# Performance work log

Hardware: AMD Instinct MI355X
Metric: run time of the kernel (lower is better)

The kernel has to match this reference:

```python
import jax, jax.numpy as jnp
import numpy as np

B, S, H, KV, D = 1, 2048, 32, 8, 128
HID = H * D
SINK, WIN, POOL = 128, 1024, 100
TAU = 1.0


def setup_inputs() -> dict:
    key = jax.random.key(0)
    ks = jax.random.split(key, 12)
    init = lambda k, shape: jax.random.normal(k, shape, jnp.float32) * 0.02
    return dict(
        hidden_states=jax.random.normal(ks[0], (B, S, HID), jnp.float32),
        Wq=init(ks[1], (HID, HID)),
        Wk=init(ks[2], (HID, KV * D)),
        Wv=init(ks[3], (HID, KV * D)),
        Wo=init(ks[4], (HID, HID)),
        fe1_w=init(ks[5], (D, 8 * D)), fe1_b=jnp.zeros((8 * D,), jnp.float32),
        fe2_w=init(ks[6], (8 * D, 2 * D)), fe2_b=jnp.zeros((2 * D,), jnp.float32),
        r1_w=init(ks[7], (2 * D, 4 * D)), r1_b=jnp.zeros((4 * D,), jnp.float32),
        r2_w=init(ks[8], (4 * D, D)), r2_b=jnp.zeros((D,), jnp.float32),
        r3_w=init(ks[9], (D, 1)), r3_b=jnp.zeros((1,), jnp.float32),
        router_noise=jax.random.uniform(ks[10], (B, 1), jnp.float32),
    )


def _rope(x):
    # x: [B,S,h,D]; non-interleaved (rotate-half) RoPE, base 10000
    half = D // 2
    inv_freq = 1.0 / (10000.0 ** (jnp.arange(0, D, 2, dtype=jnp.float32) / D))
    t = jnp.arange(S, dtype=jnp.float32)
    freqs = jnp.outer(t, inv_freq)  # [S, half]
    cos = jnp.cos(freqs)[None, :, None, :]
    sin = jnp.sin(freqs)[None, :, None, :]
    x1, x2 = x[..., :half], x[..., half:]
    return jnp.concatenate([x1 * cos - x2 * sin, x2 * cos + x1 * sin], axis=-1)


def reference(hidden_states, Wq, Wk, Wv, Wo, fe1_w, fe1_b, fe2_w, fe2_b,
              r1_w, r1_b, r2_w, r2_b, r3_w, r3_b, router_noise):
    q = (hidden_states @ Wq).reshape(B, S, H, D)
    k = (hidden_states @ Wk).reshape(B, S, KV, D)
    v = (hidden_states @ Wv).reshape(B, S, KV, D)
    q = _rope(q)
    k = _rope(k)
    # GQA: repeat kv heads
    kr = jnp.repeat(k, H // KV, axis=2)
    vr = jnp.repeat(v, H // KV, axis=2)
    scale = 1.0 / jnp.sqrt(jnp.float32(D))
    scores = jnp.einsum('bshd,bthd->bhst', q, kr) * scale  # [B,H,S,S]
    i = jnp.arange(S)[:, None]
    j = jnp.arange(S)[None, :]
    causal = j <= i
    # sink tokens + sliding window (streaming-LLM pattern)
    stream = causal & ((j < SINK) | (j > i - WIN))
    neg = jnp.float32(-1e30)
    p_full = jax.nn.softmax(jnp.where(causal, scores, neg), axis=-1)
    p_strm = jax.nn.softmax(jnp.where(stream, scores, neg), axis=-1)
    o_full = jnp.einsum('bhst,bthd->bshd', p_full, vr)
    o_strm = jnp.einsum('bhst,bthd->bshd', p_strm, vr)
    # Router: ctx_q pooling over first/last POOL query positions -> [B,H,D] -> [B,D]
    pooled = jnp.concatenate([q[:, :POOL], q[:, -POOL:]], axis=1).mean(axis=1)
    feat = pooled.mean(axis=1)  # [B,D]
    h1 = jax.nn.silu(feat @ fe1_w + fe1_b)
    h2 = h1 @ fe2_w + fe2_b
    h3 = jax.nn.silu(h2 @ r1_w + r1_b)
    h4 = jax.nn.silu(h3 @ r2_w + r2_b)
    logits = h4 @ r3_w + r3_b  # [B,1]
    eps = 1e-8
    g = -jnp.log(-jnp.log(router_noise + eps) + eps)
    z_soft = jax.nn.sigmoid((logits + g) / TAU)
    z_hard = (z_soft > 0.5).astype(z_soft.dtype)
    z = z_hard + z_soft - jax.lax.stop_gradient(z_soft)  # straight-through
    mix = z.reshape(B, 1, 1, 1)
    o = mix * o_strm + (1.0 - mix) * o_full  # gate sparse vs full retrieval
    return o.reshape(B, S, HID) @ Wo
```

## Files before the change

kernel.cpp:

```cpp
#include <hip/hip_runtime.h>
#include <hip/hip_bf16.h>

typedef unsigned short u16;
typedef unsigned int u32;
typedef __bf16 bf16x8 __attribute__((ext_vector_type(8)));
typedef float f32x4 __attribute__((ext_vector_type(4)));
typedef unsigned short u16x8 __attribute__((ext_vector_type(8)));

#define S_ 2048
#define H_ 32
#define KV_ 8
#define D_ 128
#define HID_ 4096
#define KVD_ 1024
#define QKVN 6144
#define SINK_ 128
#define WIN_ 1024
#define POOL_ 100
#define KVB 64

__device__ __forceinline__ u16 f2bf(float f) {
  union { float f; u32 u; } v; v.f = f;
  u32 r = v.u + 0x7FFFu + ((v.u >> 16) & 1u);
  return (u16)(r >> 16);
}
__device__ __forceinline__ float bf2f(u16 h) {
  union { u32 u; float f; } v; v.u = ((u32)h) << 16;
  return v.f;
}
__device__ __forceinline__ void glds16(const void* g, void* l) {
  __builtin_amdgcn_global_load_lds((__attribute__((address_space(1))) void*)g,
                                   (__attribute__((address_space(3))) void*)l, 16, 0, 0);
}

__device__ __forceinline__ void tr64(const float* __restrict__ W, u16* __restrict__ Wt,
                                     int K, int N, int nt, int kt, int tid, u16 T[64][66]) {
  const int r = tid >> 4, c4 = tid & 15;
#pragma unroll
  for (int p = 0; p < 4; ++p) {
    int row = p * 16 + r;
    float4 v = *(const float4*)&W[(size_t)(kt * 64 + row) * N + nt * 64 + c4 * 4];
    T[row][c4 * 4 + 0] = f2bf(v.x);
    T[row][c4 * 4 + 1] = f2bf(v.y);
    T[row][c4 * 4 + 2] = f2bf(v.z);
    T[row][c4 * 4 + 3] = f2bf(v.w);
  }
  __syncthreads();
  const int n = tid >> 3, c8 = tid & 7;
#pragma unroll
  for (int p = 0; p < 2; ++p) {
    int row = p * 32 + n;
    u16x8 o;
#pragma unroll
    for (int i = 0; i < 8; ++i) o[i] = T[c8 * 8 + i][row];
    *(u16x8*)&Wt[(size_t)(nt * 64 + row) * K + kt * 64 + c8 * 8] = o;
  }
}

__global__ __launch_bounds__(256) void k_prep(const float* __restrict__ hs, u16* __restrict__ hsb,
                                              const float* __restrict__ Wq, const float* __restrict__ Wk,
                                              const float* __restrict__ Wv, const float* __restrict__ Wo,
                                              u16* __restrict__ wqkv, u16* __restrict__ wot,
                                              float* __restrict__ cosT, float* __restrict__ sinT) {
  __shared__ u16 T[64][66];
  const int b = blockIdx.x, tid = threadIdx.x;
  if (b < 8192) {
    int i = b * 256 + tid;
    float4 v = ((const float4*)hs)[i];
    union { u16 s[4]; unsigned long long ll; } o;
    o.s[0] = f2bf(v.x); o.s[1] = f2bf(v.y); o.s[2] = f2bf(v.z); o.s[3] = f2bf(v.w);
    ((unsigned long long*)hsb)[i] = o.ll;
  } else if (b < 12288) {
    int id = b - 8192;
    tr64(Wq, wqkv, HID_, HID_, id % 64, id / 64, tid, T);
  } else if (b < 13312) {
    int id = b - 12288;
    tr64(Wk, wqkv + (size_t)4096 * HID_, HID_, KVD_, id % 16, id / 16, tid, T);
  } else if (b < 14336) {
    int id = b - 13312;
    tr64(Wv, wqkv + (size_t)5120 * HID_, HID_, KVD_, id % 16, id / 16, tid, T);
  } else if (b < 18432) {
    int id = b - 14336;
    tr64(Wo, wot, HID_, HID_, id % 64, id / 64, tid, T);
  } else {
    int idx = (b - 18432) * 256 + tid;
    int s = idx >> 6, i = idx & 63;
    float inv = powf(10000.f, -(float)i * (1.f / 64.f));
    float ang = (float)s * inv;
    cosT[idx] = cosf(ang);
    sinT[idx] = sinf(ang);
  }
}

__global__ __launch_bounds__(256) void k_pos(u16* __restrict__ qkv, u16* __restrict__ kro,
                                             u16* __restrict__ vt,
                                             const float* __restrict__ cosT, const float* __restrict__ sinT) {
  __shared__ u16 T[32][33];
  const int b = blockIdx.x, tid = threadIdx.x;
  if (b < 16384) {
    int idx = b * 256 + tid;
    int i = idx & 63, h = (idx >> 6) & 31, s = idx >> 11;
    size_t base = (size_t)s * QKVN + h * D_ + i;
    float x1 = bf2f(qkv[base]), x2 = bf2f(qkv[base + 64]);
    float cs = cosT[(s << 6) + i], sn = sinT[(s << 6) + i];
    qkv[base] = f2bf(x1 * cs - x2 * sn);
    qkv[base + 64] = f2bf(x2 * cs + x1 * sn);
  } else if (b < 20480) {
    int idx = (b - 16384) * 256 + tid;
    int i = idx & 63, kv = (idx >> 6) & 7, s = idx >> 9;
    float x1 = bf2f(qkv[(size_t)s * QKVN + 4096 + kv * D_ + i]);
    float x2 = bf2f(qkv[(size_t)s * QKVN + 4096 + kv * D_ + i + 64]);
    float cs = cosT[(s << 6) + i], sn = sinT[(s << 6) + i];
    size_t ob = (size_t)kv * S_ * D_ + (size_t)s * D_ + i;
    kro[ob] = f2bf(x1 * cs - x2 * sn);
    kro[ob + 64] = f2bf(x2 * cs + x1 * sn);
  } else {
    int id = b - 20480;
    int st = id & 63, dt = (id >> 6) & 3, kv = id >> 8;
    int c = tid & 31, r0 = tid >> 5;
#pragma unroll
    for (int p = 0; p < 4; ++p) {
      int r = r0 + p * 8;
      T[r][c] = qkv[(size_t)(st * 32 + r) * QKVN + 5120 + kv * D_ + dt * 32 + c];
    }
    __syncthreads();
#pragma unroll
    for (int p = 0; p < 4; ++p) {
      int r = r0 + p * 8;
      vt[(size_t)kv * D_ * S_ + (size_t)(dt * 32 + r) * S_ + st * 32 + c] = T[c][r];
    }
  }
}

__global__ void k_feat(const u16* __restrict__ q, float* __restrict__ feat) {
  int d = blockIdx.x, tid = threadIdx.x;
  float p = 0.f;
  for (int idx = tid; idx < 2 * POOL_ * H_; idx += 256) {
    int pos = idx >> 5, hh = idx & 31;
    int s = pos < POOL_ ? pos : (S_ - 2 * POOL_) + pos;
    p += bf2f(q[(size_t)s * QKVN + hh * D_ + d]);
  }
#pragma unroll
  for (int m = 1; m < 64; m <<= 1) p += __shfl_xor(p, m);
  __shared__ float red[4];
  if ((tid & 63) == 0) red[tid >> 6] = p;
  __syncthreads();
  if (tid == 0) feat[d] = (red[0] + red[1] + red[2] + red[3]) * (1.f / (2 * POOL_ * H_));
}

__global__ __launch_bounds__(256) void k_r1(const float* __restrict__ feat, const float* __restrict__ w,
                                            const float* __restrict__ b, float* __restrict__ h1) {
  __shared__ float fs[128];
  int tid = threadIdx.x;
  if (tid < 128) fs[tid] = feat[tid];
  __syncthreads();
  int o = blockIdx.x * 256 + tid;
  float a = b[o];
#pragma unroll 16
  for (int kk = 0; kk < 128; ++kk) a += fs[kk] * w[kk * 1024 + o];
  h1[o] = a / (1.f + expf(-a));
}
__global__ __launch_bounds__(256) void k_r2(const float* __restrict__ h1, const float* __restrict__ w,
                                            float* __restrict__ h2p) {
  __shared__ float hs[64];
  int tid = threadIdx.x, b = blockIdx.x;
  if (tid < 64) hs[tid] = h1[b * 64 + tid];
  __syncthreads();
  const float* wb = w + (size_t)b * 64 * 256 + tid;
  float p = 0.f;
#pragma unroll 16
  for (int kk = 0; kk < 64; ++kk) p += hs[kk] * wb[(size_t)kk * 256];
  h2p[b * 256 + tid] = p;
}
__global__ __launch_bounds__(256) void k_r3(const float* __restrict__ h2p, const float* __restrict__ b2,
                                            const float* __restrict__ w, const float* __restrict__ b3,
                                            float* __restrict__ h3) {
  __shared__ float h2s[256];
  int tid = threadIdx.x;
  float s = b2[tid];
#pragma unroll
  for (int j = 0; j < 16; ++j) s += h2p[j * 256 + tid];
  h2s[tid] = s;
  __syncthreads();
  int o = blockIdx.x * 256 + tid;
  float a = b3[o];
#pragma unroll 16
  for (int kk = 0; kk < 256; ++kk) a += h2s[kk] * w[kk * 512 + o];
  h3[o] = a / (1.f + expf(-a));
}
__global__ __launch_bounds__(256) void k_r45(const float* __restrict__ h3, const float* __restrict__ w4,
                                             const float* __restrict__ b4, const float* __restrict__ w5,
                                             const float* __restrict__ b5, const float* __restrict__ noise,
                                             float* __restrict__ mix) {
  __shared__ float h3s[512];
  __shared__ float hp[256];
  int tid = threadIdx.x;
  h3s[tid] = h3[tid];
  h3s[tid + 256] = h3[tid + 256];
  __syncthreads();
  int t = tid & 127, half = tid >> 7;
  float a = half ? 0.f : b4[t];
  const float* wcol = w4 + (size_t)(half << 8) * 128 + t;
  const float* hbase = h3s + (half << 8);
#pragma unroll 16
  for (int i = 0; i < 256; ++i) a += hbase[i] * wcol[(size_t)i * 128];
  hp[tid] = a;
  __syncthreads();
  if (tid < 128) {
    float v = hp[tid] + hp[tid + 128];
    float h4 = v / (1.f + expf(-v));
    hp[tid] = h4 * w5[tid];
  }
  __syncthreads();
  if (tid < 64) {
    float s = hp[tid] + hp[tid + 64];
#pragma unroll
    for (int m = 32; m >= 1; m >>= 1) s += __shfl_down(s, m);
    if (tid == 0) {
      float logits = s + b5[0];
      float u = noise[0];
      float g = -logf(-logf(u + 1e-8f) + 1e-8f);
      float zs = 1.f / (1.f + expf(-(logits + g)));
      mix[0] = zs > 0.5f ? 1.f : 0.f;
    }
  }
}

template <int MFRAG, int NFRAG>
__device__ __forceinline__ void stage_u(const u16* __restrict__ A, const u16* __restrict__ Bt,
                                        u16* buf, int m0, int n0, int K, int kg, int unit, int tid) {
  constexpr int AU = MFRAG / 2;
  constexpr int BM = MFRAG * 32;
  if (unit < AU) {
    int cell = unit * 512 + tid;
    int row = cell >> 3, c = cell & 7;
    glds16(A + (size_t)(m0 + row) * K + kg + ((c ^ (row & 7)) * 8),
           buf + ((size_t)(unit * 512 + (tid & ~63))) * 8);
  } else {
    int cell = (unit - AU) * 512 + tid;
    int row = cell >> 3, c = cell & 7;
    glds16(Bt + (size_t)(n0 + row) * K + kg + ((c ^ (row & 7)) * 8),
           buf + (size_t)BM * 64 + ((size_t)((unit - AU) * 512 + (tid & ~63))) * 8);
  }
}

template <int MFRAG, int NFRAG, int OUTF32>
__global__ __launch_bounds__(512, 1) void gemm_dp(const u16* __restrict__ A, const u16* __restrict__ Bt,
                                                  void* __restrict__ C, int M, int N, int K, int NTN) {
  constexpr int BM = MFRAG * 32;
  constexpr int BN = NFRAG * 64;
  constexpr int NH = NFRAG / 2;
  constexpr int U = MFRAG / 2 + NFRAG;
  static_assert(U == 8 || U == 6, "stage schedule assumes 6 or 8 units");
  constexpr int TE = (BM + BN) * 64;
  __shared__ __align__(16) u16 lds[2 * TE];
  const int tid = threadIdx.x, w = tid >> 6, ln = tid & 63;
  const int lr = ln & 15, lk = ln >> 4;
  const int wr = w >> 2, wc = w & 3;
  const int nwg = gridDim.x, cpx = nwg >> 3;
  const int wg = (blockIdx.x & 7) * cpx + (blockIdx.x >> 3);
  const int m0 = (wg / NTN) * BM, n0 = (wg % NTN) * BN;
  f32x4 acc[MFRAG][NFRAG];
#pragma unroll
  for (int i = 0; i < MFRAG; ++i)
#pragma unroll
    for (int j = 0; j < NFRAG; ++j) acc[i][j] = (f32x4){0.f, 0.f, 0.f, 0.f};
  const int nt = K / 64;

  auto ldA = [&](const u16* buf, bf16x8* af, int kh) {
#pragma unroll
    for (int mf = 0; mf < MFRAG; ++mf) {
      int row = wr * (MFRAG * 16) + mf * 16 + lr;
      af[mf] = *(const bf16x8*)&buf[row * 64 + (((kh * 4 + lk) ^ (row & 7)) * 8)];
    }
  };
  auto ldB = [&](const u16* buf, bf16x8* bp, int kh, int nh) {
#pragma unroll
    for (int nf = 0; nf < NH; ++nf) {
      int brow = wc * (NFRAG * 16) + (nh * NH + nf) * 16 + lr;
      bp[nf] = *(const bf16x8*)&buf[BM * 64 + brow * 64 + (((kh * 4 + lk) ^ (brow & 7)) * 8)];
    }
  };
  auto MMA = [&](const bf16x8* af, const bf16x8* bp, int nh) {
    __builtin_amdgcn_s_setprio(1);
#pragma unroll
    for (int mf = 0; mf < MFRAG; ++mf)
#pragma unroll
      for (int nf = 0; nf < NH; ++nf)
        acc[mf][nh * NH + nf] =
            __builtin_amdgcn_mfma_f32_16x16x32_bf16(af[mf], bp[nf], acc[mf][nh * NH + nf], 0, 0, 0);
    __builtin_amdgcn_s_setprio(0);
  };

#pragma unroll
  for (int i = 0; i < U; ++i) stage_u<MFRAG, NFRAG>(A, Bt, lds, m0, n0, K, 0, i, tid);
  stage_u<MFRAG, NFRAG>(A, Bt, lds + TE, m0, n0, K, 64, 0, tid);
  stage_u<MFRAG, NFRAG>(A, Bt, lds + TE, m0, n0, K, 64, 1, tid);
  asm volatile("s_waitcnt vmcnt(2)" ::: "memory");
  asm volatile("s_barrier" ::: "memory");
  bf16x8 afA[MFRAG], afB[MFRAG], b0[NH], b1[NH];
  ldA(lds, afA, 0);
  ldB(lds, b0, 0, 0);

  for (int t = 0; t < nt; ++t) {
    const u16* cb = lds + (t & 1) * TE;
    u16* nb = lds + ((t + 1) & 1) * TE;
    const bool hn = (t + 1 < nt);
    const int kn = (t + 1) * 64;
    asm volatile("s_barrier" ::: "memory");
    MMA(afA, b0, 0);
    ldB(cb, b1, 0, 1);
    if (hn) {
      stage_u<MFRAG, NFRAG>(A, Bt, nb, m0, n0, K, kn, 2, tid);
      stage_u<MFRAG, NFRAG>(A, Bt, nb, m0, n0, K, kn, 3, tid);
    }
    asm volatile("s_barrier" ::: "memory");
    MMA(afA, b1, 1);
    ldA(cb, afB, 1);
    ldB(cb, b0, 1, 0);
    if (hn) {
      stage_u<MFRAG, NFRAG>(A, Bt, nb, m0, n0, K, kn, 4, tid);
      stage_u<MFRAG, NFRAG>(A, Bt, nb, m0, n0, K, kn, 5, tid);
    }
    asm volatile("s_barrier" ::: "memory");
    MMA(afB, b0, 0);
    ldB(cb, b1, 1, 1);
    if (hn && U == 8) {
      stage_u<MFRAG, NFRAG>(A, Bt, nb, m0, n0, K, kn, 6, tid);
      stage_u<MFRAG, NFRAG>(A, Bt, nb, m0, n0, K, kn, 7, tid);
    }
    asm volatile("s_barrier" ::: "memory");
    MMA(afB, b1, 1);
    asm volatile("s_barrier" ::: "memory");
    if (hn) {
      if (t + 2 < nt) {
        stage_u<MFRAG, NFRAG>(A, Bt, (u16*)cb, m0, n0, K, (t + 2) * 64, 0, tid);
        stage_u<MFRAG, NFRAG>(A, Bt, (u16*)cb, m0, n0, K, (t + 2) * 64, 1, tid);
        asm volatile("s_waitcnt vmcnt(2)" ::: "memory");
      } else {
        asm volatile("s_waitcnt vmcnt(0)" ::: "memory");
      }
      asm volatile("s_barrier" ::: "memory");
      ldA(nb, afA, 0);
      ldB(nb, b0, 0, 0);
    }
  }
#pragma unroll
  for (int mf = 0; mf < MFRAG; ++mf) {
    int row = m0 + wr * (MFRAG * 16) + mf * 16 + lk * 4;
#pragma unroll
    for (int nf = 0; nf < NFRAG; ++nf) {
      int col = n0 + wc * (NFRAG * 16) + nf * 16 + lr;
#pragma unroll
      for (int jj = 0; jj < 4; ++jj) {
        float v = acc[mf][nf][jj];
        if (OUTF32) ((float*)C)[(size_t)(row + jj) * N + col] = v;
        else ((u16*)C)[(size_t)(row + jj) * N + col] = f2bf(v);
      }
    }
  }
}

__global__ __launch_bounds__(256) void k_attn(const u16* __restrict__ q, const u16* __restrict__ kr,
                                              const u16* __restrict__ vt, u16* __restrict__ o,
                                              const float* __restrict__ mixp, int qs) {
  __shared__ __align__(16) u16 Ks[2][KVB * 128];
  __shared__ __align__(16) u16 Vs[2][128 * KVB];
  __shared__ __align__(16) u16 Ps[4][16 * KVB];
  const int tid = threadIdx.x, w = tid >> 6, ln = tid & 63;
  const int lr = ln & 15, lk = ln >> 4;
  const int bid = blockIdx.x;
  const int qblk = (S_ / 64 - 1) - (bid >> 5);
  const int h = bid & 31, kv = h >> 2;
  const bool strm = (*mixp) > 0.5f;
  const int q0 = qblk * 64;
  const int qrow = q0 + w * 16 + lr;
  bf16x8 qf[4];
#pragma unroll
  for (int c = 0; c < 4; ++c)
    qf[c] = *(const bf16x8*)(q + (size_t)qrow * qs + h * D_ + c * 32 + lk * 8);
  f32x4 oacc[8];
#pragma unroll
  for (int c = 0; c < 8; ++c) oacc[c] = (f32x4){0.f, 0.f, 0.f, 0.f};
  float mrun[4], lrun[4];
#pragma unroll
  for (int j = 0; j < 4; ++j) { mrun[j] = -1e30f; lrun[j] = 0.f; }
  const u16* kbase = kr + (size_t)kv * S_ * D_;
  const u16* vbase = vt + (size_t)kv * D_ * S_;
  const int qg0 = q0 + w * 16 + lk * 4;
  const float scale = 0.08838834764831845f;

  auto stage = [&](int kt, int b) {
    const int kb0 = kt * KVB;
#pragma unroll
    for (int c = 0; c < 4; ++c) {
      int r0 = c * 16 + w * 4;
      int rg = r0 + (ln >> 4);
      int cg = (ln & 15) ^ (rg & 7);
      glds16(kbase + (size_t)(kb0 + rg) * D_ + cg * 8, &Ks[b][r0 * 128]);
    }
#pragma unroll
    for (int c = 0; c < 4; ++c) {
      int r0 = c * 32 + w * 8;
      int rg = r0 + (ln >> 3);
      int cg = (ln & 7) ^ (rg & 7);
      glds16(vbase + (size_t)rg * S_ + kb0 + cg * 8, &Vs[b][r0 * KVB]);
    }
  };
  auto nxt = [&](int k) {
    ++k;
    if (strm)
      while (k <= qblk && k * KVB >= SINK_ && k * KVB + KVB - 1 + WIN_ <= q0) ++k;
    return k;
  };

  int kt = 0, buf = 0;
  stage(0, 0);
  int ktn = nxt(0);
  while (kt <= qblk) {
    const bool hn = (ktn <= qblk);
    if (hn) {
      stage(ktn, buf ^ 1);
      asm volatile("s_waitcnt vmcnt(8)" ::: "memory");
    } else {
      asm volatile("s_waitcnt vmcnt(0)" ::: "memory");
    }
    asm volatile("s_barrier" ::: "memory");
    const int kb0 = kt * KVB;
    const u16* ks = Ks[buf];
    const u16* vs = Vs[buf];
    f32x4 sg[4];
#pragma unroll
    for (int g = 0; g < 4; ++g) sg[g] = (f32x4){0.f, 0.f, 0.f, 0.f};
    __builtin_amdgcn_s_setprio(1);
#pragma unroll
    for (int g = 0; g < 4; ++g) {
      int krow = g * 16 + lr;
      int sw = krow & 7;
#pragma unroll
      for (int c = 0; c < 4; ++c) {
        bf16x8 kf = *(const bf16x8*)&ks[krow * 128 + (((c * 4 + lk) ^ sw) * 8)];
        sg[g] = __builtin_amdgcn_mfma_f32_16x16x32_bf16(qf[c], kf, sg[g], 0, 0, 0);
      }
    }
    __builtin_amdgcn_s_setprio(0);
    const bool lastt = (kt == qblk);
    const bool needm = lastt ||
        (strm && !(kb0 + KVB <= SINK_ || kb0 >= q0 + 64 - WIN_));
    if (needm) {
#pragma unroll
      for (int g = 0; g < 4; ++g) {
        int kg = kb0 + g * 16 + lr;
#pragma unroll
        for (int j = 0; j < 4; ++j) {
          int qi = qg0 + j;
          float v = sg[g][j] * scale;
          bool ok = (kg <= qi) && (!strm || kg < SINK_ || kg > qi - WIN_);
          sg[g][j] = ok ? v : -1e30f;
        }
      }
    } else {
#pragma unroll
      for (int g = 0; g < 4; ++g)
#pragma unroll
        for (int j = 0; j < 4; ++j) sg[g][j] *= scale;
    }
    float rmax[4];
#pragma unroll
    for (int j = 0; j < 4; ++j)
      rmax[j] = fmaxf(fmaxf(sg[0][j], sg[1][j]), fmaxf(sg[2][j], sg[3][j]));
#pragma unroll
    for (int m2 = 1; m2 < 16; m2 <<= 1)
#pragma unroll
      for (int j = 0; j < 4; ++j) rmax[j] = fmaxf(rmax[j], __shfl_xor(rmax[j], m2));
    float dmax = rmax[0] - mrun[0];
#pragma unroll
    for (int j = 1; j < 4; ++j) dmax = fmaxf(dmax, rmax[j] - mrun[j]);
    if (!__all(dmax <= 8.f)) {
      float corr[4];
#pragma unroll
      for (int j = 0; j < 4; ++j) {
        float mn = fmaxf(mrun[j], rmax[j]);
        corr[j] = __expf(mrun[j] - mn);
        mrun[j] = mn;
        lrun[j] *= corr[j];
      }
#pragma unroll
      for (int c = 0; c < 8; ++c) {
        f32x4 t2 = oacc[c];
        t2[0] *= corr[0]; t2[1] *= corr[1]; t2[2] *= corr[2]; t2[3] *= corr[3];
        oacc[c] = t2;
      }
    }
    float rsum[4] = {0.f, 0.f, 0.f, 0.f};
#pragma unroll
    for (int g = 0; g < 4; ++g)
#pragma unroll
      for (int j = 0; j < 4; ++j) {
        float p = __expf(sg[g][j] - mrun[j]);
        sg[g][j] = p;
        rsum[j] += p;
      }
#pragma unroll
    for (int m2 = 1; m2 < 16; m2 <<= 1)
#pragma unroll
      for (int j = 0; j < 4; ++j) rsum[j] += __shfl_xor(rsum[j], m2);
#pragma unroll
    for (int j = 0; j < 4; ++j) lrun[j] += rsum[j];
#pragma unroll
    for (int g = 0; g < 4; ++g) {
      int col = g * 16 + lr;
      int c16 = col >> 3;
#pragma unroll
      for (int j = 0; j < 4; ++j) {
        int row = lk * 4 + j;
        Ps[w][row * KVB + ((c16 ^ (row & 7)) * 8) + (col & 7)] = f2bf(sg[g][j]);
      }
    }
    __builtin_amdgcn_s_setprio(1);
#pragma unroll
    for (int half = 0; half < 2; ++half) {
      bf16x8 pf = *(const bf16x8*)&Ps[w][lr * KVB + (((half * 4 + lk) ^ (lr & 7)) * 8)];
#pragma unroll
      for (int cc = 0; cc < 8; ++cc) {
        int vrow = cc * 16 + lr;
        bf16x8 vf = *(const bf16x8*)&vs[vrow * KVB + (((half * 4 + lk) ^ (vrow & 7)) * 8)];
        oacc[cc] = __builtin_amdgcn_mfma_f32_16x16x32_bf16(pf, vf, oacc[cc], 0, 0, 0);
      }
    }
    __builtin_amdgcn_s_setprio(0);
    asm volatile("s_barrier" ::: "memory");
    kt = ktn;
    ktn = nxt(ktn);
    buf ^= 1;
  }
#pragma unroll
  for (int cc = 0; cc < 8; ++cc)
#pragma unroll
    for (int j = 0; j < 4; ++j) {
      float ov = oacc[cc][j] / lrun[j];
      o[(size_t)(qg0 + j) * HID_ + h * D_ + cc * 16 + lr] = f2bf(ov);
    }
}

extern "C" void kernel_launch(void* const* d_in, const int* in_sizes, int n_in,
                              void* d_out, int out_size, void* d_ws, size_t ws_size,
                              hipStream_t stream) {
  const float* hs = (const float*)d_in[0];
  const float* Wq = (const float*)d_in[1];
  const float* Wk = (const float*)d_in[2];
  const float* Wv = (const float*)d_in[3];
  const float* Wo = (const float*)d_in[4];
  const float* fe1_w = (const float*)d_in[5];
  const float* fe1_b = (const float*)d_in[6];
  const float* fe2_w = (const float*)d_in[7];
  const float* fe2_b = (const float*)d_in[8];
  const float* r1_w = (const float*)d_in[9];
  const float* r1_b = (const float*)d_in[10];
  const float* r2_w = (const float*)d_in[11];
  const float* r2_b = (const float*)d_in[12];
  const float* r3_w = (const float*)d_in[13];
  const float* r3_b = (const float*)d_in[14];
  const float* noise = (const float*)d_in[15];

  char* ws = (char*)d_ws;
  size_t off = 0;
  auto alloc = [&](size_t b) { char* p = ws + off; off += (b + 255) & ~(size_t)255; return p; };
  u16* hsb = (u16*)alloc((size_t)S_ * HID_ * 2);
  u16* wqkv = (u16*)alloc((size_t)QKVN * HID_ * 2);
  u16* qkvbuf = (u16*)alloc((size_t)S_ * QKVN * 2);
  u16* wot = (u16*)alloc((size_t)HID_ * HID_ * 2);
  u16* krbuf = (u16*)alloc((size_t)S_ * KVD_ * 2);
  u16* vtbuf = (u16*)alloc((size_t)S_ * KVD_ * 2);
  u16* obuf = (u16*)alloc((size_t)S_ * HID_ * 2);
  float* cosT = (float*)alloc((size_t)S_ * 64 * 4);
  float* sinT = (float*)alloc((size_t)S_ * 64 * 4);
  float* feat = (float*)alloc(512);
  float* mix = (float*)alloc(256);
  float* h1buf = (float*)alloc(1024 * 4);
  float* h2p = (float*)alloc(16 * 256 * 4);
  float* h3buf = (float*)alloc(512 * 4);

  k_prep<<<dim3(18944), dim3(256), 0, stream>>>(hs, hsb, Wq, Wk, Wv, Wo, wqkv, wot, cosT, sinT);

  gemm_dp<4, 6, 0><<<dim3(256), dim3(512), 0, stream>>>(hsb, wqkv, (void*)qkvbuf,
                                                        S_, QKVN, HID_, QKVN / 384);

  k_pos<<<dim3(22528), dim3(256), 0, stream>>>(qkvbuf, krbuf, vtbuf, cosT, sinT);

  k_feat<<<dim3(D_), dim3(256), 0, stream>>>(qkvbuf, feat);
  k_r1<<<dim3(4), dim3(256), 0, stream>>>(feat, fe1_w, fe1_b, h1buf);
  k_r2<<<dim3(16), dim3(256), 0, stream>>>(h1buf, fe2_w, h2p);
  k_r3<<<dim3(2), dim3(256), 0, stream>>>(h2p, fe2_b, r1_w, r1_b, h3buf);
  k_r45<<<dim3(1), dim3(256), 0, stream>>>(h3buf, r2_w, r2_b, r3_w, r3_b, noise, mix);

  k_attn<<<dim3((S_ / 64) * H_), dim3(256), 0, stream>>>(qkvbuf, krbuf, vtbuf, obuf, mix, QKVN);

  gemm_dp<4, 4, 1><<<dim3(256), dim3(512), 0, stream>>>(obuf, wot, d_out,
                                                        S_, HID_, HID_, HID_ / 256);
}
```

Baseline: 366.0 us.

## Prefetch full next-next K tile after compute instead of interleaving loads

The GEMM main loop used to spread the global-to-LDS loads for tile t+1 across the four MMA phases and stage only two units of tile t+2 at the end. Now every unit of tile t+2 is issued in one batch after the MMAs finish, and the wait is vmcnt(U), so the loads have a whole iteration to land. The aim is a clean two-tile-deep prefetch that hides global memory latency better. The cost is that load issue is no longer interleaved with MFMA work, which bunches memory traffic and could leave the loads competing with LDS reads at the iteration boundary.

```diff
diff --git a/kernel.cpp b/kernel.cpp
--- a/kernel.cpp
+++ b/kernel.cpp
@@ -251,7 +251,7 @@
   constexpr int BN = NFRAG * 64;
   constexpr int NH = NFRAG / 2;
   constexpr int U = MFRAG / 2 + NFRAG;
-  static_assert(U == 8 || U == 6, "stage schedule assumes 6 or 8 units");
+  static_assert(U == 8 || U == 6, "vmcnt immediates assume 6 or 8 units");
   constexpr int TE = (BM + BN) * 64;
   __shared__ __align__(16) u16 lds[2 * TE];
   const int tid = threadIdx.x, w = tid >> 6, ln = tid & 63;
@@ -291,12 +291,16 @@
             __builtin_amdgcn_mfma_f32_16x16x32_bf16(af[mf], bp[nf], acc[mf][nh * NH + nf], 0, 0, 0);
     __builtin_amdgcn_s_setprio(0);
   };
+  auto wait_u = [&]() {
+    if constexpr (U == 8) asm volatile("s_waitcnt vmcnt(8)" ::: "memory");
+    else asm volatile("s_waitcnt vmcnt(6)" ::: "memory");
+  };
 
 #pragma unroll
   for (int i = 0; i < U; ++i) stage_u<MFRAG, NFRAG>(A, Bt, lds, m0, n0, K, 0, i, tid);
-  stage_u<MFRAG, NFRAG>(A, Bt, lds + TE, m0, n0, K, 64, 0, tid);
-  stage_u<MFRAG, NFRAG>(A, Bt, lds + TE, m0, n0, K, 64, 1, tid);
-  asm volatile("s_waitcnt vmcnt(2)" ::: "memory");
+#pragma unroll
+  for (int i = 0; i < U; ++i) stage_u<MFRAG, NFRAG>(A, Bt, lds + TE, m0, n0, K, 64, i, tid);
+  wait_u();
   asm volatile("s_barrier" ::: "memory");
   bf16x8 afA[MFRAG], afB[MFRAG], b0[NH], b1[NH];
   ldA(lds, afA, 0);
@@ -306,37 +310,25 @@
     const u16* cb = lds + (t & 1) * TE;
     u16* nb = lds + ((t + 1) & 1) * TE;
     const bool hn = (t + 1 < nt);
-    const int kn = (t + 1) * 64;
     asm volatile("s_barrier" ::: "memory");
     MMA(afA, b0, 0);
     ldB(cb, b1, 0, 1);
-    if (hn) {
-      stage_u<MFRAG, NFRAG>(A, Bt, nb, m0, n0, K, kn, 2, tid);
-      stage_u<MFRAG, NFRAG>(A, Bt, nb, m0, n0, K, kn, 3, tid);
-    }
     asm volatile("s_barrier" ::: "memory");
     MMA(afA, b1, 1);
     ldA(cb, afB, 1);
     ldB(cb, b0, 1, 0);
-    if (hn) {
-      stage_u<MFRAG, NFRAG>(A, Bt, nb, m0, n0, K, kn, 4, tid);
-      stage_u<MFRAG, NFRAG>(A, Bt, nb, m0, n0, K, kn, 5, tid);
-    }
     asm volatile("s_barrier" ::: "memory");
     MMA(afB, b0, 0);
     ldB(cb, b1, 1, 1);
-    if (hn && U == 8) {
-      stage_u<MFRAG, NFRAG>(A, Bt, nb, m0, n0, K, kn, 6, tid);
-      stage_u<MFRAG, NFRAG>(A, Bt, nb, m0, n0, K, kn, 7, tid);
-    }
     asm volatile("s_barrier" ::: "memory");
     MMA(afB, b1, 1);
     asm volatile("s_barrier" ::: "memory");
     if (hn) {
       if (t + 2 < nt) {
-        stage_u<MFRAG, NFRAG>(A, Bt, (u16*)cb, m0, n0, K, (t + 2) * 64, 0, tid);
-        stage_u<MFRAG, NFRAG>(A, Bt, (u16*)cb, m0, n0, K, (t + 2) * 64, 1, tid);
-        asm volatile("s_waitcnt vmcnt(2)" ::: "memory");
+#pragma unroll
+        for (int i = 0; i < U; ++i)
+          stage_u<MFRAG, NFRAG>(A, Bt, (u16*)cb, m0, n0, K, (t + 2) * 64, i, tid);
+        wait_u();
       } else {
         asm volatile("s_waitcnt vmcnt(0)" ::: "memory");
       }
```

New measurement: 374.3 us. 1.02x slower.

## Shrink GEMM tiles to 64-row blocks with K=32 steps and two blocks per CU

Applied to the files above, without the earlier changes.

Rewrites the projection GEMM kernel to use 64xBN tiles with 4 waves (256 threads) and a K-step of 32 instead of 128xBN tiles with 8 waves and K-step 64. It adds a new LDS swizzle for the 32-wide rows and launches twice as many workgroups so two can share a CU. The aim is more occupancy and better load balance across CUs. The cost is less operand reuse per tile, twice as many barriers per unit of K, and more global traffic for the A matrix.

```diff
diff --git a/kernel.cpp b/kernel.cpp
--- a/kernel.cpp
+++ b/kernel.cpp
@@ -226,65 +226,62 @@
   }
 }
 
-template <int MFRAG, int NFRAG>
+template <int NFRAG>
 __device__ __forceinline__ void stage_u(const u16* __restrict__ A, const u16* __restrict__ Bt,
                                         u16* buf, int m0, int n0, int K, int kg, int unit, int tid) {
-  constexpr int AU = MFRAG / 2;
-  constexpr int BM = MFRAG * 32;
-  if (unit < AU) {
-    int cell = unit * 512 + tid;
-    int row = cell >> 3, c = cell & 7;
-    glds16(A + (size_t)(m0 + row) * K + kg + ((c ^ (row & 7)) * 8),
-           buf + ((size_t)(unit * 512 + (tid & ~63))) * 8);
+  if (unit == 0) {
+    int row = tid >> 2, c = tid & 3;
+    int cg = c ^ ((row >> 1) & 3);
+    glds16(A + (size_t)(m0 + row) * K + kg + cg * 8,
+           buf + ((size_t)(tid & ~63)) * 8);
   } else {
-    int cell = (unit - AU) * 512 + tid;
-    int row = cell >> 3, c = cell & 7;
-    glds16(Bt + (size_t)(n0 + row) * K + kg + ((c ^ (row & 7)) * 8),
-           buf + (size_t)BM * 64 + ((size_t)((unit - AU) * 512 + (tid & ~63))) * 8);
-  }
-}
-
-template <int MFRAG, int NFRAG, int OUTF32>
-__global__ __launch_bounds__(512, 1) void gemm_dp(const u16* __restrict__ A, const u16* __restrict__ Bt,
+    int cell = (unit - 1) * 256 + tid;
+    int row = cell >> 2, c = cell & 3;
+    int cg = c ^ ((row >> 1) & 3);
+    glds16(Bt + (size_t)(n0 + row) * K + kg + cg * 8,
+           buf + 2048 + ((size_t)((unit - 1) * 256 + (tid & ~63))) * 8);
+  }
+}
+
+template <int NFRAG, int OUTF32>
+__global__ __launch_bounds__(256, 2) void gemm_dp(const u16* __restrict__ A, const u16* __restrict__ Bt,
                                                   void* __restrict__ C, int M, int N, int K, int NTN) {
-  constexpr int BM = MFRAG * 32;
   constexpr int BN = NFRAG * 64;
   constexpr int NH = NFRAG / 2;
-  constexpr int U = MFRAG / 2 + NFRAG;
-  static_assert(U == 8 || U == 6, "stage schedule assumes 6 or 8 units");
-  constexpr int TE = (BM + BN) * 64;
+  constexpr int U = 1 + NFRAG;
+  constexpr int TE = (64 + BN) * 32;
   __shared__ __align__(16) u16 lds[2 * TE];
   const int tid = threadIdx.x, w = tid >> 6, ln = tid & 63;
   const int lr = ln & 15, lk = ln >> 4;
-  const int wr = w >> 2, wc = w & 3;
+  const int wc = w;
   const int nwg = gridDim.x, cpx = nwg >> 3;
   const int wg = (blockIdx.x & 7) * cpx + (blockIdx.x >> 3);
-  const int m0 = (wg / NTN) * BM, n0 = (wg % NTN) * BN;
-  f32x4 acc[MFRAG][NFRAG];
-#pragma unroll
-  for (int i = 0; i < MFRAG; ++i)
+  const int m0 = (wg / NTN) * 64, n0 = (wg % NTN) * BN;
+  f32x4 acc[4][NFRAG];
+#pragma unroll
+  for (int i = 0; i < 4; ++i)
 #pragma unroll
     for (int j = 0; j < NFRAG; ++j) acc[i][j] = (f32x4){0.f, 0.f, 0.f, 0.f};
-  const int nt = K / 64;
-
-  auto ldA = [&](const u16* buf, bf16x8* af, int kh) {
-#pragma unroll
-    for (int mf = 0; mf < MFRAG; ++mf) {
-      int row = wr * (MFRAG * 16) + mf * 16 + lr;
-      af[mf] = *(const bf16x8*)&buf[row * 64 + (((kh * 4 + lk) ^ (row & 7)) * 8)];
+  const int nt = K / 32;
+
+  auto ldA = [&](const u16* buf, bf16x8* af) {
+#pragma unroll
+    for (int mf = 0; mf < 4; ++mf) {
+      int row = mf * 16 + lr;
+      af[mf] = *(const bf16x8*)&buf[row * 32 + ((lk ^ ((row >> 1) & 3)) * 8)];
     }
   };
-  auto ldB = [&](const u16* buf, bf16x8* bp, int kh, int nh) {
+  auto ldB = [&](const u16* buf, bf16x8* bp, int nh) {
 #pragma unroll
     for (int nf = 0; nf < NH; ++nf) {
       int brow = wc * (NFRAG * 16) + (nh * NH + nf) * 16 + lr;
-      bp[nf] = *(const bf16x8*)&buf[BM * 64 + brow * 64 + (((kh * 4 + lk) ^ (brow & 7)) * 8)];
+      bp[nf] = *(const bf16x8*)&buf[2048 + brow * 32 + ((lk ^ ((brow >> 1) & 3)) * 8)];
     }
   };
   auto MMA = [&](const bf16x8* af, const bf16x8* bp, int nh) {
     __builtin_amdgcn_s_setprio(1);
 #pragma unroll
-    for (int mf = 0; mf < MFRAG; ++mf)
+    for (int mf = 0; mf < 4; ++mf)
 #pragma unroll
       for (int nf = 0; nf < NH; ++nf)
         acc[mf][nh * NH + nf] =
@@ -293,61 +290,55 @@
   };
 
 #pragma unroll
-  for (int i = 0; i < U; ++i) stage_u<MFRAG, NFRAG>(A, Bt, lds, m0, n0, K, 0, i, tid);
-  stage_u<MFRAG, NFRAG>(A, Bt, lds + TE, m0, n0, K, 64, 0, tid);
-  stage_u<MFRAG, NFRAG>(A, Bt, lds + TE, m0, n0, K, 64, 1, tid);
-  asm volatile("s_waitcnt vmcnt(2)" ::: "memory");
+  for (int i = 0; i < U; ++i) stage_u<NFRAG>(A, Bt, lds, m0, n0, K, 0, i, tid);
+  stage_u<NFRAG>(A, Bt, lds + TE, m0, n0, K, 32, 0, tid);
+  asm volatile("s_waitcnt vmcnt(1)" ::: "memory");
   asm volatile("s_barrier" ::: "memory");
-  bf16x8 afA[MFRAG], afB[MFRAG], b0[NH], b1[NH];
-  ldA(lds, afA, 0);
-  ldB(lds, b0, 0, 0);
+  bf16x8 afA[4], b0[NH], b1[NH];
+  ldA(lds, afA);
+  ldB(lds, b0, 0);
 
   for (int t = 0; t < nt; ++t) {
     const u16* cb = lds + (t & 1) * TE;
     u16* nb = lds + ((t + 1) & 1) * TE;
     const bool hn = (t + 1 < nt);
-    const int kn = (t + 1) * 64;
+    const int kn = (t + 1) * 32;
     asm volatile("s_barrier" ::: "memory");
     MMA(afA, b0, 0);
-    ldB(cb, b1, 0, 1);
+    ldB(cb, b1, 1);
     if (hn) {
-      stage_u<MFRAG, NFRAG>(A, Bt, nb, m0, n0, K, kn, 2, tid);
-      stage_u<MFRAG, NFRAG>(A, Bt, nb, m0, n0, K, kn, 3, tid);
+      stage_u<NFRAG>(A, Bt, nb, m0, n0, K, kn, 1, tid);
+      stage_u<NFRAG>(A, Bt, nb, m0, n0, K, kn, 2, tid);
+      if (NFRAG == 6) stage_u<NFRAG>(A, Bt, nb, m0, n0, K, kn, 3, tid);
     }
     asm volatile("s_barrier" ::: "memory");
     MMA(afA, b1, 1);
-    ldA(cb, afB, 1);
-    ldB(cb, b0, 1, 0);
     if (hn) {
-      stage_u<MFRAG, NFRAG>(A, Bt, nb, m0, n0, K, kn, 4, tid);
-      stage_u<MFRAG, NFRAG>(A, Bt, nb, m0, n0, K, kn, 5, tid);
-    }
-    asm volatile("s_barrier" ::: "memory");
-    MMA(afB, b0, 0);
-    ldB(cb, b1, 1, 1);
-    if (hn && U == 8) {
-      stage_u<MFRAG, NFRAG>(A, Bt, nb, m0, n0, K, kn, 6, tid);
-      stage_u<MFRAG, NFRAG>(A, Bt, nb, m0, n0, K, kn, 7, tid);
-    }
-    asm volatile("s_barrier" ::: "memory");
-    MMA(afB, b1, 1);
+      if (NFRAG == 6) {
+        stage_u<NFRAG>(A, Bt, nb, m0, n0, K, kn, 4, tid);
+        stage_u<NFRAG>(A, Bt, nb, m0, n0, K, kn, 5, tid);
+        stage_u<NFRAG>(A, Bt, nb, m0, n0, K, kn, 6, tid);
+      } else {
+        stage_u<NFRAG>(A, Bt, nb, m0, n0, K, kn, 3, tid);
+        stage_u<NFRAG>(A, Bt, nb, m0, n0, K, kn, 4, tid);
+      }
+    }
     asm volatile("s_barrier" ::: "memory");
     if (hn) {
       if (t + 2 < nt) {
-        stage_u<MFRAG, NFRAG>(A, Bt, (u16*)cb, m0, n0, K, (t + 2) * 64, 0, tid);
-        stage_u<MFRAG, NFRAG>(A, Bt, (u16*)cb, m0, n0, K, (t + 2) * 64, 1, tid);
-        asm volatile("s_waitcnt vmcnt(2)" ::: "memory");
+        stage_u<NFRAG>(A, Bt, (u16*)cb, m0, n0, K, (t + 2) * 32, 0, tid);
+        asm volatile("s_waitcnt vmcnt(1)" ::: "memory");
       } else {
         asm volatile("s_waitcnt vmcnt(0)" ::: "memory");
       }
       asm volatile("s_barrier" ::: "memory");
-      ldA(nb, afA, 0);
-      ldB(nb, b0, 0, 0);
-    }
-  }
-#pragma unroll
-  for (int mf = 0; mf < MFRAG; ++mf) {
-    int row = m0 + wr * (MFRAG * 16) + mf * 16 + lk * 4;
+      ldA(nb, afA);
+      ldB(nb, b0, 0);
+    }
+  }
+#pragma unroll
+  for (int mf = 0; mf < 4; ++mf) {
+    int row = m0 + mf * 16 + lk * 4;
 #pragma unroll
     for (int nf = 0; nf < NFRAG; ++nf) {
       int col = n0 + wc * (NFRAG * 16) + nf * 16 + lr;
@@ -583,8 +574,8 @@
 
   k_prep<<<dim3(18944), dim3(256), 0, stream>>>(hs, hsb, Wq, Wk, Wv, Wo, wqkv, wot, cosT, sinT);
 
-  gemm_dp<4, 6, 0><<<dim3(256), dim3(512), 0, stream>>>(hsb, wqkv, (void*)qkvbuf,
-                                                        S_, QKVN, HID_, QKVN / 384);
+  gemm_dp<6, 0><<<dim3(512), dim3(256), 0, stream>>>(hsb, wqkv, (void*)qkvbuf,
+                                                     S_, QKVN, HID_, QKVN / 384);
 
   k_pos<<<dim3(22528), dim3(256), 0, stream>>>(qkvbuf, krbuf, vtbuf, cosT, sinT);
 
@@ -596,6 +587,6 @@
 
   k_attn<<<dim3((S_ / 64) * H_), dim3(256), 0, stream>>>(qkvbuf, krbuf, vtbuf, obuf, mix, QKVN);
 
-  gemm_dp<4, 4, 1><<<dim3(256), dim3(512), 0, stream>>>(obuf, wot, d_out,
-                                                        S_, HID_, HID_, HID_ / 256);
-}
+  gemm_dp<4, 1><<<dim3(512), dim3(256), 0, stream>>>(obuf, wot, d_out,
+                                                     S_, HID_, HID_, HID_ / 256);
+}
```

Measured after the change: 431.4 us. 1.18x slower.
